# Optimization experiments

Measured on AMD Instinct MI355X. Metric: run time of the kernel, lower is better.

The kernel has to match this reference:

```python
import jax, jax.numpy as jnp
import numpy as np
import math

D_MODEL = 1024
N_HEADS = 16
HEAD_DIM = D_MODEL // N_HEADS
BATCH = 2
SEQ = 2048


def setup_inputs() -> dict:
    key = jax.random.key(0)
    ks = jax.random.split(key, 6)
    x = jax.random.normal(ks[0], (BATCH, SEQ, D_MODEL), dtype=jnp.float32)
    # causal additive mask, finite large negative
    causal = jnp.tril(jnp.ones((SEQ, SEQ), dtype=bool))
    attn_mask = jnp.where(causal, 0.0, -1e9).astype(jnp.float32)[None, None, :, :]
    s = 1.0 / math.sqrt(D_MODEL)
    W_qkv = jax.random.uniform(ks[1], (3 * D_MODEL, D_MODEL), jnp.float32, -s, s)
    b_qkv = jax.random.uniform(ks[2], (3 * D_MODEL,), jnp.float32, -s, s)
    W_out = jax.random.uniform(ks[3], (D_MODEL, D_MODEL), jnp.float32, -s, s)
    b_out = jax.random.uniform(ks[4], (D_MODEL,), jnp.float32, -s, s)
    return {"x": x, "attn_mask": attn_mask, "W_qkv": W_qkv, "b_qkv": b_qkv,
            "W_out": W_out, "b_out": b_out}


def reference(x, attn_mask, W_qkv, b_qkv, W_out, b_out):
    batch, seq, _ = x.shape
    # torch Linear: x @ W^T + b
    qkv = x @ W_qkv.T + b_qkv                              # [B,S,3D]
    qkv = qkv.reshape(batch, seq, 3, N_HEADS, HEAD_DIM)
    qkv = jnp.transpose(qkv, (2, 0, 3, 1, 4))              # [3,B,H,S,hd]
    q, k, v = qkv[0], qkv[1], qkv[2]
    scores = jnp.einsum('bhsd,bhtd->bhst', q, k) / math.sqrt(HEAD_DIM)
    scores = scores + attn_mask
    attn = jax.nn.softmax(scores, axis=-1)                 # dropout p=0 (eval)
    context = jnp.einsum('bhst,bhtd->bhsd', attn, v)       # [B,H,S,hd]
    context = jnp.transpose(context, (0, 2, 1, 3)).reshape(batch, seq, D_MODEL)
    return context @ W_out.T + b_out
```

## Files before the change

### kernel.cpp

```cpp
#include <hip/hip_runtime.h>
#include <hip/hip_bf16.h>

#define BATCH 2
#define SEQ 2048
#define DMODEL 1024
#define NHEADS 16
#define HDIM 64
#define MROWS (BATCH*SEQ)

typedef short bf16x8_t __attribute__((ext_vector_type(8)));
typedef float f32x4_t __attribute__((ext_vector_type(4)));

union Frag { uint4 u; bf16x8_t b; };

__device__ __forceinline__ unsigned short f2bf(float f) {
  union { __hip_bfloat16 h; unsigned short s; } u;
  u.h = __float2bfloat16(f);
  return u.s;
}

__device__ __forceinline__ void gload16(const unsigned short* g, unsigned short* l) {
  __builtin_amdgcn_global_load_lds(
      (const __attribute__((address_space(1))) unsigned int*)(const void*)g,
      (__attribute__((address_space(3))) unsigned int*)(void*)l,
      16, 0, 0);
}

__global__ void cvt3_kernel(const float* __restrict__ a, const float* __restrict__ b,
                            const float* __restrict__ c,
                            unsigned short* __restrict__ oa, unsigned short* __restrict__ ob,
                            unsigned short* __restrict__ oc,
                            int na, int nb, int nc) {
  const int n = na + nb + nc;
  for (int i = blockIdx.x * blockDim.x + threadIdx.x; i < n;
       i += gridDim.x * blockDim.x) {
    const float* src; unsigned short* dst; int j;
    if (i < na)           { src = a; dst = oa; j = i; }
    else if (i < na + nb) { src = b; dst = ob; j = i - na; }
    else                  { src = c; dst = oc; j = i - na - nb; }
    float4 v = reinterpret_cast<const float4*>(src)[j];
    ushort4 o;
    o.x = f2bf(v.x); o.y = f2bf(v.y); o.z = f2bf(v.z); o.w = f2bf(v.w);
    reinterpret_cast<ushort4*>(dst)[j] = o;
  }
}

#define QSCALE 0.18033688011112042f

__device__ __forceinline__ int xcd_swizzle(int bid, int nwg) {
  return (bid & 7) * (nwg >> 3) + (bid >> 3);
}


__launch_bounds__(256)
__global__ void qkv_gemm_kernel(const unsigned short* __restrict__ A,
                                const unsigned short* __restrict__ Bw,
                                const float* __restrict__ bias,
                                unsigned short* __restrict__ qb,
                                unsigned short* __restrict__ kb,
                                unsigned short* __restrict__ vb) {
  __shared__ __align__(16) unsigned short As[128 * 32];
  __shared__ __align__(16) unsigned short Bs[128 * 32];
  const int tid = threadIdx.x;
  const int w = tid >> 6, lane = tid & 63;
  const int rr = lane & 15, cg = lane >> 4;
  const int wr = w >> 1, wc = w & 1;

  const int nwg = gridDim.x * gridDim.y;
  const int swz = xcd_swizzle(blockIdx.y * gridDim.x + blockIdx.x, nwg);
  const int bm = (swz % gridDim.x) * 128, bn = (swz / gridDim.x) * 128;

  const int cid0 = (w * 2) * 64 + lane, cid1 = (w * 2 + 1) * 64 + lane;
  const int rowA0 = cid0 >> 2, kc0 = cid0 & 3;
  const int rowA1 = cid1 >> 2, kc1 = cid1 & 3;
  const unsigned short* gA0 = A + (size_t)(bm + rowA0) * DMODEL + kc0 * 8;
  const unsigned short* gA1 = A + (size_t)(bm + rowA1) * DMODEL + kc1 * 8;
  const unsigned short* gB0 = Bw + (size_t)(bn + rowA0) * DMODEL + kc0 * 8;
  const unsigned short* gB1 = Bw + (size_t)(bn + rowA1) * DMODEL + kc1 * 8;
  unsigned short* lA0 = As + (w * 2) * 512;
  unsigned short* lA1 = As + (w * 2 + 1) * 512;
  unsigned short* lB0 = Bs + (w * 2) * 512;
  unsigned short* lB1 = Bs + (w * 2 + 1) * 512;

  f32x4_t acc[4][4];
#pragma unroll
  for (int i = 0; i < 4; ++i)
#pragma unroll
    for (int j = 0; j < 4; ++j) acc[i][j] = (f32x4_t){0.f, 0.f, 0.f, 0.f};

  for (int k0 = 0; k0 < DMODEL; k0 += 32) {
    __syncthreads();
    gload16(gA0 + k0, lA0);
    gload16(gA1 + k0, lA1);
    gload16(gB0 + k0, lB0);
    gload16(gB1 + k0, lB1);
    __syncthreads();
    const uint4* A4 = reinterpret_cast<const uint4*>(As);
    const uint4* B4 = reinterpret_cast<const uint4*>(Bs);
    Frag af[4], bf[4];
#pragma unroll
    for (int mt = 0; mt < 4; ++mt) af[mt].u = A4[(wr * 64 + 16 * mt + rr) * 4 + cg];
#pragma unroll
    for (int nt = 0; nt < 4; ++nt) bf[nt].u = B4[(wc * 64 + 16 * nt + rr) * 4 + cg];
#pragma unroll
    for (int mt = 0; mt < 4; ++mt)
#pragma unroll
      for (int nt = 0; nt < 4; ++nt)
        acc[mt][nt] = __builtin_amdgcn_mfma_f32_16x16x32_bf16(af[mt].b, bf[nt].b, acc[mt][nt], 0, 0, 0);
  }

#pragma unroll
  for (int nt = 0; nt < 4; ++nt) {
    const int m = bn + wc * 64 + 16 * nt + rr;
    const float bv = bias[m];
    const int which = m >> 10;
    const int h = (m & 1023) >> 6;
    const int d = m & 63;
#pragma unroll
    for (int mt = 0; mt < 4; ++mt) {
#pragma unroll
      for (int r = 0; r < 4; ++r) {
        const int n = bm + wr * 64 + 16 * mt + cg * 4 + r;
        const int b = n >> 11, sq = n & (SEQ - 1);
        const int bh = b * NHEADS + h;
        float val = acc[mt][nt][r] + bv;
        if (which == 0) {
          qb[((size_t)bh * SEQ + sq) * HDIM + d] = f2bf(val * QSCALE);
        } else if (which == 1) {
          kb[((size_t)bh * SEQ + sq) * HDIM + d] = f2bf(val);
        } else {
          vb[((size_t)bh * HDIM + d) * SEQ + sq] = f2bf(val);
        }
      }
    }
  }
}

__launch_bounds__(256)
__global__ void out_gemm_kernel(const unsigned short* __restrict__ A,
                                const unsigned short* __restrict__ Bw,
                                const float* __restrict__ bias,
                                float* __restrict__ out) {
  __shared__ __align__(16) unsigned short As[128 * 32];
  __shared__ __align__(16) unsigned short Bs[128 * 32];
  const int tid = threadIdx.x;
  const int w = tid >> 6, lane = tid & 63;
  const int rr = lane & 15, cg = lane >> 4;
  const int wr = w >> 1, wc = w & 1;

  const int nwg = gridDim.x * gridDim.y;
  const int swz = xcd_swizzle(blockIdx.y * gridDim.x + blockIdx.x, nwg);
  const int bm = (swz % gridDim.x) * 128, bn = (swz / gridDim.x) * 128;

  const int cid0 = (w * 2) * 64 + lane, cid1 = (w * 2 + 1) * 64 + lane;
  const int rowA0 = cid0 >> 2, kc0 = cid0 & 3;
  const int rowA1 = cid1 >> 2, kc1 = cid1 & 3;
  const unsigned short* gA0 = A + (size_t)(bm + rowA0) * DMODEL + kc0 * 8;
  const unsigned short* gA1 = A + (size_t)(bm + rowA1) * DMODEL + kc1 * 8;
  const unsigned short* gB0 = Bw + (size_t)(bn + rowA0) * DMODEL + kc0 * 8;
  const unsigned short* gB1 = Bw + (size_t)(bn + rowA1) * DMODEL + kc1 * 8;
  unsigned short* lA0 = As + (w * 2) * 512;
  unsigned short* lA1 = As + (w * 2 + 1) * 512;
  unsigned short* lB0 = Bs + (w * 2) * 512;
  unsigned short* lB1 = Bs + (w * 2 + 1) * 512;

  f32x4_t acc[4][4];
#pragma unroll
  for (int i = 0; i < 4; ++i)
#pragma unroll
    for (int j = 0; j < 4; ++j) acc[i][j] = (f32x4_t){0.f, 0.f, 0.f, 0.f};

  for (int k0 = 0; k0 < DMODEL; k0 += 32) {
    __syncthreads();
    gload16(gA0 + k0, lA0);
    gload16(gA1 + k0, lA1);
    gload16(gB0 + k0, lB0);
    gload16(gB1 + k0, lB1);
    __syncthreads();
    const uint4* A4 = reinterpret_cast<const uint4*>(As);
    const uint4* B4 = reinterpret_cast<const uint4*>(Bs);
    Frag af[4], bf[4];
#pragma unroll
    for (int mt = 0; mt < 4; ++mt) af[mt].u = A4[(wr * 64 + 16 * mt + rr) * 4 + cg];
#pragma unroll
    for (int nt = 0; nt < 4; ++nt) bf[nt].u = B4[(wc * 64 + 16 * nt + rr) * 4 + cg];
#pragma unroll
    for (int mt = 0; mt < 4; ++mt)
#pragma unroll
      for (int nt = 0; nt < 4; ++nt)
        acc[mt][nt] = __builtin_amdgcn_mfma_f32_16x16x32_bf16(af[mt].b, bf[nt].b, acc[mt][nt], 0, 0, 0);
  }

#pragma unroll
  for (int nt = 0; nt < 4; ++nt) {
    const int m = bn + wc * 64 + 16 * nt + rr;
    const float bv = bias[m];
#pragma unroll
    for (int mt = 0; mt < 4; ++mt) {
#pragma unroll
      for (int r = 0; r < 4; ++r) {
        const int n = bm + wr * 64 + 16 * mt + cg * 4 + r;
        out[(size_t)n * DMODEL + m] = acc[mt][nt][r] + bv;
      }
    }
  }
}

__launch_bounds__(256, 4)
__global__ void attn_kernel(const unsigned short* __restrict__ qb,
                            const unsigned short* __restrict__ kb,
                            const unsigned short* __restrict__ vb,
                            unsigned short* __restrict__ ctx) {
  __shared__ __align__(16) uint4 Ks[2][512];
  __shared__ __align__(16) uint4 Vs[2][512];

  const int tid = threadIdx.x;
  const int w = tid >> 6, lane = tid & 63;
  const int rr = lane & 15, cg = lane >> 4;
  const int rxw = rr & 7;
  const int bh = blockIdx.x;
  const int c = 31 - blockIdx.y;

  const unsigned short* Kbh = kb + (size_t)bh * SEQ * HDIM;
  const unsigned short* Vbh = vb + (size_t)bh * HDIM * SEQ;

  const int j0 = w * 2, j1 = w * 2 + 1;
  const int cid0 = j0 * 64 + lane, cid1 = j1 * 64 + lane;
  const int row0 = cid0 >> 3, ch0 = cid0 & 7;
  const int row1 = cid1 >> 3, ch1 = cid1 & 7;
  const int kOff0 = row0 * HDIM + ((ch0 ^ (row0 & 7)) << 3);
  const int kOff1 = row1 * HDIM + ((ch1 ^ (row1 & 7)) << 3);
  const int vOff0 = row0 * SEQ + ((ch0 ^ (row0 & 7)) << 3);
  const int vOff1 = row1 * SEQ + ((ch1 ^ (row1 & 7)) << 3);

#define STAGE(bi, tb_) do {                                             \
    const unsigned short* Kt_ = Kbh + (size_t)(tb_) * HDIM;             \
    const unsigned short* Vt_ = Vbh + (tb_);                            \
    unsigned short* kl_ = (unsigned short*)&Ks[bi][0];                  \
    unsigned short* vl_ = (unsigned short*)&Vs[bi][0];                  \
    gload16(Kt_ + kOff0, kl_ + j0 * 512);                               \
    gload16(Kt_ + kOff1, kl_ + j1 * 512);                               \
    gload16(Vt_ + vOff0, vl_ + j0 * 512);                               \
    gload16(Vt_ + vOff1, vl_ + j1 * 512);                               \
  } while (0)

  const int b = bh >> 4, h = bh & 15;
  const int s_base = c * 64 + w * 16;
  const int nt = c + 1;

  STAGE(0, 0);

  Frag q0, q1;
  {
    const unsigned short* qrow = qb + ((size_t)bh * SEQ + (s_base + rr)) * HDIM;
    q0.u = *reinterpret_cast<const uint4*>(qrow + cg * 8);
    q1.u = *reinterpret_cast<const uint4*>(qrow + 32 + cg * 8);
  }

  f32x4_t acc[4];
#pragma unroll
  for (int i = 0; i < 4; ++i) acc[i] = (f32x4_t){0.f, 0.f, 0.f, 0.f};
  float mreg = -1e30f;
  float lp = 0.f;

  for (int t = 0; t < nt; ++t) {
    __syncthreads();
    if (t + 1 < nt) STAGE((t + 1) & 1, (t + 1) * 64);
    const uint4* Kt = &Ks[t & 1][0];
    const uint4* Vt = &Vs[t & 1][0];

    f32x4_t s[4];
    __builtin_amdgcn_s_setprio(1);
#pragma unroll
    for (int st = 0; st < 4; ++st) {
      s[st] = (f32x4_t){0.f, 0.f, 0.f, 0.f};
      Frag kf;
      kf.u = Kt[(st * 16 + rr) * 8 + (cg ^ rxw)];
      s[st] = __builtin_amdgcn_mfma_f32_16x16x32_bf16(kf.b, q0.b, s[st], 0, 0, 0);
      kf.u = Kt[(st * 16 + rr) * 8 + ((4 + cg) ^ rxw)];
      s[st] = __builtin_amdgcn_mfma_f32_16x16x32_bf16(kf.b, q1.b, s[st], 0, 0, 0);
    }
    __builtin_amdgcn_s_setprio(0);

    if (t == nt - 1) {
#pragma unroll
      for (int st = 0; st < 4; ++st)
#pragma unroll
        for (int r = 0; r < 4; ++r)
          if (st * 16 + cg * 4 + r > w * 16 + rr) s[st][r] = -1e30f;
    }

    float mx = s[0][0];
#pragma unroll
    for (int st = 0; st < 4; ++st)
#pragma unroll
      for (int r = 0; r < 4; ++r) mx = fmaxf(mx, s[st][r]);
    if (__any(mx > mreg + 11.0f)) {
      float m = fmaxf(mx, __shfl_xor(mx, 16));
      m = fmaxf(m, __shfl_xor(m, 32));
      m = fmaxf(m, mreg);
      const float alpha = exp2f(mreg - m);
      mreg = m;
      lp *= alpha;
      float av[4];
#pragma unroll
      for (int r = 0; r < 4; ++r) av[r] = __shfl(alpha, cg * 4 + r);
#pragma unroll
      for (int dt = 0; dt < 4; ++dt)
#pragma unroll
        for (int r = 0; r < 4; ++r) acc[dt][r] *= av[r];
    }

    float pv[4][4];
#pragma unroll
    for (int st = 0; st < 4; ++st)
#pragma unroll
      for (int r = 0; r < 4; ++r) {
        pv[st][r] = exp2f(s[st][r] - mreg);
        lp += pv[st][r];
      }

    unsigned int uu[4][2];
#pragma unroll
    for (int st = 0; st < 4; ++st)
#pragma unroll
      for (int i = 0; i < 2; ++i)
        asm("v_cvt_pk_bf16_f32 %0, %1, %2"
            : "=v"(uu[st][i]) : "v"(pv[st][2 * i]), "v"(pv[st][2 * i + 1]));

    Frag pA0, pA1;
#pragma unroll
    for (int s2 = 0; s2 < 2; ++s2) {
#pragma unroll
      for (int i = 0; i < 2; ++i) {
        unsigned int x = uu[2 * s2][i], y = uu[2 * s2 + 1][i];
        asm("v_permlane32_swap_b32 %0, %1" : "+v"(x), "+v"(y));
        asm("v_permlane16_swap_b32 %0, %1" : "+v"(x), "+v"(y));
        if (s2 == 0) { pA0.u[i] = x; pA0.u[2 + i] = y; }
        else         { pA1.u[i] = x; pA1.u[2 + i] = y; }
      }
    }

    __builtin_amdgcn_s_setprio(1);
#pragma unroll
    for (int dt = 0; dt < 4; ++dt) {
      Frag vf;
      vf.u = Vt[(dt * 16 + rr) * 8 + (cg ^ rxw)];
      acc[dt] = __builtin_amdgcn_mfma_f32_16x16x32_bf16(pA0.b, vf.b, acc[dt], 0, 0, 0);
      vf.u = Vt[(dt * 16 + rr) * 8 + ((4 + cg) ^ rxw)];
      acc[dt] = __builtin_amdgcn_mfma_f32_16x16x32_bf16(pA1.b, vf.b, acc[dt], 0, 0, 0);
    }
    __builtin_amdgcn_s_setprio(0);
  }

  float ls = lp + __shfl_xor(lp, 16);
  ls += __shfl_xor(ls, 32);
  const float inv = 1.0f / ls;
  float iv[4];
#pragma unroll
  for (int r = 0; r < 4; ++r) iv[r] = __shfl(inv, cg * 4 + r);
#pragma unroll
  for (int r = 0; r < 4; ++r) {
    const int sq = s_base + cg * 4 + r;
    unsigned short* crow = ctx + (size_t)(b * SEQ + sq) * DMODEL + h * HDIM;
#pragma unroll
    for (int dt = 0; dt < 4; ++dt)
      crow[dt * 16 + rr] = f2bf(acc[dt][r] * iv[r]);
  }
#undef STAGE
}

extern "C" void kernel_launch(void* const* d_in, const int* in_sizes, int n_in,
                              void* d_out, int out_size, void* d_ws, size_t ws_size,
                              hipStream_t stream) {
  const float* x    = (const float*)d_in[0];
  const float* Wqkv = (const float*)d_in[2];
  const float* bqkv = (const float*)d_in[3];
  const float* Wout = (const float*)d_in[4];
  const float* bout = (const float*)d_in[5];
  float* out = (float*)d_out;

  unsigned short* ws    = (unsigned short*)d_ws;
  unsigned short* xb    = ws;
  unsigned short* wqkvb = xb + (size_t)MROWS * DMODEL;
  unsigned short* woutb = wqkvb + (size_t)3 * DMODEL * DMODEL;
  unsigned short* qbuf  = woutb + (size_t)DMODEL * DMODEL;
  unsigned short* kbuf  = qbuf + (size_t)BATCH * NHEADS * SEQ * HDIM;
  unsigned short* vbuf  = kbuf + (size_t)BATCH * NHEADS * SEQ * HDIM;
  unsigned short* ctx   = vbuf + (size_t)BATCH * NHEADS * SEQ * HDIM;

  cvt3_kernel<<<2048, 256, 0, stream>>>(
      x, Wqkv, Wout, xb, wqkvb, woutb,
      MROWS * DMODEL / 4, 3 * DMODEL * DMODEL / 4, DMODEL * DMODEL / 4);

  qkv_gemm_kernel<<<dim3(MROWS / 128, 3 * DMODEL / 128), 256, 0, stream>>>(
      xb, wqkvb, bqkv, qbuf, kbuf, vbuf);

  attn_kernel<<<dim3(BATCH * NHEADS, SEQ / 64), 256, 0, stream>>>(
      qbuf, kbuf, vbuf, ctx);

  out_gemm_kernel<<<dim3(MROWS / 128, DMODEL / 128), 256, 0, stream>>>(
      ctx, woutb, bout, out);
}
```

Baseline: 126.6 us.

## Double-buffer LDS in projection GEMMs, drop XCD swizzle, raise MFMA priority

Both projection GEMMs now use two LDS stages. The next K-tile's global-to-LDS load is issued right after the barrier, while the MFMAs run on the current tile, and one of the two barriers per iteration is removed. The XCD block-index swizzle is dropped in favour of plain blockIdx mapping, and s_setprio brackets the MFMA block. The aim is to hide global load latency behind compute, at the cost of doubling LDS use and possibly losing L2 locality from the removed swizzle.

Result: faster. 117.1 us (-7.5%).

```diff
diff --git a/kernel.cpp b/kernel.cpp
--- a/kernel.cpp
+++ b/kernel.cpp
@@ -47,10 +47,6 @@
 
 #define QSCALE 0.18033688011112042f
 
-__device__ __forceinline__ int xcd_swizzle(int bid, int nwg) {
-  return (bid & 7) * (nwg >> 3) + (bid >> 3);
-}
-
 
 __launch_bounds__(256)
 __global__ void qkv_gemm_kernel(const unsigned short* __restrict__ A,
@@ -59,16 +55,13 @@
                                 unsigned short* __restrict__ qb,
                                 unsigned short* __restrict__ kb,
                                 unsigned short* __restrict__ vb) {
-  __shared__ __align__(16) unsigned short As[128 * 32];
-  __shared__ __align__(16) unsigned short Bs[128 * 32];
+  __shared__ __align__(16) unsigned short As[2 * 128 * 32];
+  __shared__ __align__(16) unsigned short Bs[2 * 128 * 32];
   const int tid = threadIdx.x;
   const int w = tid >> 6, lane = tid & 63;
   const int rr = lane & 15, cg = lane >> 4;
   const int wr = w >> 1, wc = w & 1;
-
-  const int nwg = gridDim.x * gridDim.y;
-  const int swz = xcd_swizzle(blockIdx.y * gridDim.x + blockIdx.x, nwg);
-  const int bm = (swz % gridDim.x) * 128, bn = (swz / gridDim.x) * 128;
+  const int bm = blockIdx.x * 128, bn = blockIdx.y * 128;
 
   const int cid0 = (w * 2) * 64 + lane, cid1 = (w * 2 + 1) * 64 + lane;
   const int rowA0 = cid0 >> 2, kc0 = cid0 & 3;
@@ -82,32 +75,39 @@
   unsigned short* lB0 = Bs + (w * 2) * 512;
   unsigned short* lB1 = Bs + (w * 2 + 1) * 512;
 
+#define GSTAGE(bi_, k0_) do {                       \
+    gload16(gA0 + (k0_), lA0 + (bi_) * 4096);       \
+    gload16(gA1 + (k0_), lA1 + (bi_) * 4096);       \
+    gload16(gB0 + (k0_), lB0 + (bi_) * 4096);       \
+    gload16(gB1 + (k0_), lB1 + (bi_) * 4096);       \
+  } while (0)
+
   f32x4_t acc[4][4];
 #pragma unroll
   for (int i = 0; i < 4; ++i)
 #pragma unroll
     for (int j = 0; j < 4; ++j) acc[i][j] = (f32x4_t){0.f, 0.f, 0.f, 0.f};
 
-  for (int k0 = 0; k0 < DMODEL; k0 += 32) {
+  GSTAGE(0, 0);
+  for (int it = 0; it < DMODEL / 32; ++it) {
     __syncthreads();
-    gload16(gA0 + k0, lA0);
-    gload16(gA1 + k0, lA1);
-    gload16(gB0 + k0, lB0);
-    gload16(gB1 + k0, lB1);
-    __syncthreads();
-    const uint4* A4 = reinterpret_cast<const uint4*>(As);
-    const uint4* B4 = reinterpret_cast<const uint4*>(Bs);
+    if (it + 1 < DMODEL / 32) GSTAGE((it + 1) & 1, (it + 1) * 32);
+    const uint4* A4 = reinterpret_cast<const uint4*>(As) + (it & 1) * 512;
+    const uint4* B4 = reinterpret_cast<const uint4*>(Bs) + (it & 1) * 512;
     Frag af[4], bf[4];
 #pragma unroll
     for (int mt = 0; mt < 4; ++mt) af[mt].u = A4[(wr * 64 + 16 * mt + rr) * 4 + cg];
 #pragma unroll
     for (int nt = 0; nt < 4; ++nt) bf[nt].u = B4[(wc * 64 + 16 * nt + rr) * 4 + cg];
+    __builtin_amdgcn_s_setprio(1);
 #pragma unroll
     for (int mt = 0; mt < 4; ++mt)
 #pragma unroll
       for (int nt = 0; nt < 4; ++nt)
         acc[mt][nt] = __builtin_amdgcn_mfma_f32_16x16x32_bf16(af[mt].b, bf[nt].b, acc[mt][nt], 0, 0, 0);
-  }
+    __builtin_amdgcn_s_setprio(0);
+  }
+#undef GSTAGE
 
 #pragma unroll
   for (int nt = 0; nt < 4; ++nt) {
@@ -141,16 +141,13 @@
                                 const unsigned short* __restrict__ Bw,
                                 const float* __restrict__ bias,
                                 float* __restrict__ out) {
-  __shared__ __align__(16) unsigned short As[128 * 32];
-  __shared__ __align__(16) unsigned short Bs[128 * 32];
+  __shared__ __align__(16) unsigned short As[2 * 128 * 32];
+  __shared__ __align__(16) unsigned short Bs[2 * 128 * 32];
   const int tid = threadIdx.x;
   const int w = tid >> 6, lane = tid & 63;
   const int rr = lane & 15, cg = lane >> 4;
   const int wr = w >> 1, wc = w & 1;
-
-  const int nwg = gridDim.x * gridDim.y;
-  const int swz = xcd_swizzle(blockIdx.y * gridDim.x + blockIdx.x, nwg);
-  const int bm = (swz % gridDim.x) * 128, bn = (swz / gridDim.x) * 128;
+  const int bm = blockIdx.x * 128, bn = blockIdx.y * 128;
 
   const int cid0 = (w * 2) * 64 + lane, cid1 = (w * 2 + 1) * 64 + lane;
   const int rowA0 = cid0 >> 2, kc0 = cid0 & 3;
@@ -164,32 +161,39 @@
   unsigned short* lB0 = Bs + (w * 2) * 512;
   unsigned short* lB1 = Bs + (w * 2 + 1) * 512;
 
+#define GSTAGE(bi_, k0_) do {                       \
+    gload16(gA0 + (k0_), lA0 + (bi_) * 4096);       \
+    gload16(gA1 + (k0_), lA1 + (bi_) * 4096);       \
+    gload16(gB0 + (k0_), lB0 + (bi_) * 4096);       \
+    gload16(gB1 + (k0_), lB1 + (bi_) * 4096);       \
+  } while (0)
+
   f32x4_t acc[4][4];
 #pragma unroll
   for (int i = 0; i < 4; ++i)
 #pragma unroll
     for (int j = 0; j < 4; ++j) acc[i][j] = (f32x4_t){0.f, 0.f, 0.f, 0.f};
 
-  for (int k0 = 0; k0 < DMODEL; k0 += 32) {
+  GSTAGE(0, 0);
+  for (int it = 0; it < DMODEL / 32; ++it) {
     __syncthreads();
-    gload16(gA0 + k0, lA0);
-    gload16(gA1 + k0, lA1);
-    gload16(gB0 + k0, lB0);
-    gload16(gB1 + k0, lB1);
-    __syncthreads();
-    const uint4* A4 = reinterpret_cast<const uint4*>(As);
-    const uint4* B4 = reinterpret_cast<const uint4*>(Bs);
+    if (it + 1 < DMODEL / 32) GSTAGE((it + 1) & 1, (it + 1) * 32);
+    const uint4* A4 = reinterpret_cast<const uint4*>(As) + (it & 1) * 512;
+    const uint4* B4 = reinterpret_cast<const uint4*>(Bs) + (it & 1) * 512;
     Frag af[4], bf[4];
 #pragma unroll
     for (int mt = 0; mt < 4; ++mt) af[mt].u = A4[(wr * 64 + 16 * mt + rr) * 4 + cg];
 #pragma unroll
     for (int nt = 0; nt < 4; ++nt) bf[nt].u = B4[(wc * 64 + 16 * nt + rr) * 4 + cg];
+    __builtin_amdgcn_s_setprio(1);
 #pragma unroll
     for (int mt = 0; mt < 4; ++mt)
 #pragma unroll
       for (int nt = 0; nt < 4; ++nt)
         acc[mt][nt] = __builtin_amdgcn_mfma_f32_16x16x32_bf16(af[mt].b, bf[nt].b, acc[mt][nt], 0, 0, 0);
-  }
+    __builtin_amdgcn_s_setprio(0);
+  }
+#undef GSTAGE
 
 #pragma unroll
   for (int nt = 0; nt < 4; ++nt) {
```
